# Kernel tuning notes

Hardware: AMD Instinct MI355X
Metric: run time of the kernel (lower is better)

Reference implementation:

```python
import jax, jax.numpy as jnp
import numpy as np

N_NODES = 200000
N_EDGES = 500000
F_IN = 165
HIDDEN = 384
OUT = 2


def setup_inputs() -> dict:
    key = jax.random.key(0)
    ks = jax.random.split(key, 8)
    x = jax.random.normal(ks[0], (N_NODES, F_IN), dtype=jnp.float32)
    edge_index = jax.random.randint(ks[1], (2, N_EDGES), 0, N_NODES, dtype=jnp.int64)
    # Glorot-ish init for GCNConv weights, zero bias (PyG default)
    def glorot(k, fan_in, fan_out):
        lim = (6.0 / (fan_in + fan_out)) ** 0.5
        return jax.random.uniform(k, (fan_in, fan_out), dtype=jnp.float32, minval=-lim, maxval=lim)
    W1 = glorot(ks[2], F_IN, HIDDEN)
    b1 = jnp.zeros((HIDDEN,), dtype=jnp.float32)
    W2 = glorot(ks[3], HIDDEN, HIDDEN)
    b2 = jnp.zeros((HIDDEN,), dtype=jnp.float32)
    W3 = glorot(ks[4], HIDDEN, OUT)
    b3 = jnp.zeros((OUT,), dtype=jnp.float32)
    return {"x": x, "edge_index": edge_index,
            "W1": W1, "b1": b1, "W2": W2, "b2": b2, "W3": W3, "b3": b3}


def _gcn_norm(edge_index, num_nodes):
    # PyG gcn_norm: add self-loops, symmetric normalization D^-1/2 (A+I) D^-1/2
    loop = jnp.arange(num_nodes, dtype=edge_index.dtype)
    row = jnp.concatenate([edge_index[0], loop])
    col = jnp.concatenate([edge_index[1], loop])
    ones = jnp.ones(row.shape[0], dtype=jnp.float32)
    deg = jax.ops.segment_sum(ones, col, num_segments=num_nodes)
    dinv = jnp.where(deg > 0, jax.lax.rsqrt(deg), 0.0)
    norm = dinv[row] * dinv[col]  # [E + N]
    return row, col, norm


def _gcn_conv(h, W, b, row, col, norm, num_nodes):
    h = h @ W                          # [N, F_out] linear transform first
    msg = h[row] * norm[:, None]       # gather + scale, [E+N, F_out]
    agg = jax.ops.segment_sum(msg, col, num_segments=num_nodes)
    return agg + b


def reference(x, edge_index, W1, b1, W2, b2, W3, b3):
    n = x.shape[0]
    row, col, norm = _gcn_norm(edge_index, n)
    h = jax.nn.relu(_gcn_conv(x, W1, b1, row, col, norm, n))
    h = jax.nn.relu(_gcn_conv(h, W2, b2, row, col, norm, n))
    return _gcn_conv(h, W3, b3, row, col, norm, n)
```

## Files before the change

### kernel.cpp

```cpp
#include <hip/hip_runtime.h>
#include <hip/hip_bf16.h>

#define N_NODES 200000
#define N_EDGES 500000
#define F_IN    165
#define HIDDEN  384
#define F_OUT   2

#define KPAD1   192
#define M_TILES 1563
#define M_PAD   (M_TILES * 128)
#define NB_SCAN 782
#define GRID_GEMM (196 * 24)

typedef unsigned short ushort_t;
typedef unsigned int   uint_t;

using bf16x8 = __attribute__((ext_vector_type(8))) short;
using f32x4  = __attribute__((ext_vector_type(4))) float;

__device__ __forceinline__ float bf2f(uint_t u) {
    return __uint_as_float(u << 16);
}
__device__ __forceinline__ ushort_t f2bf(float x) {
    uint_t b = __float_as_uint(x);
    return (ushort_t)((b + 0x7FFFu + ((b >> 16) & 1u)) >> 16);
}

__device__ __forceinline__ void async16(const ushort_t* g, ushort_t* l) {
    __builtin_amdgcn_global_load_lds(
        (const __attribute__((address_space(1))) void*)g,
        (__attribute__((address_space(3))) void*)l,
        16, 0, 0);
}

__global__ void count_kernel(const int* __restrict__ col, int* __restrict__ cnt, int E) {
    int e = blockIdx.x * blockDim.x + threadIdx.x;
    if (e < E) atomicAdd(&cnt[col[e]], 1);
}

__global__ void dinv_kernel(const int* __restrict__ cnt, float* __restrict__ dinv, int n) {
    int i = blockIdx.x * blockDim.x + threadIdx.x;
    if (i < n) dinv[i] = rsqrtf((float)(cnt[i] + 1));
}

__global__ __launch_bounds__(256) void scan1_kernel(const int* __restrict__ cnt,
                                                    int* __restrict__ loc,
                                                    int* __restrict__ bsum, int N) {
    __shared__ int sh[256];
    int t = threadIdx.x;
    int i = blockIdx.x * 256 + t;
    int v = (i < N) ? cnt[i] : 0;
    sh[t] = v;
    __syncthreads();
    #pragma unroll
    for (int off = 1; off < 256; off <<= 1) {
        int u = (t >= off) ? sh[t - off] : 0;
        __syncthreads();
        sh[t] += u;
        __syncthreads();
    }
    int incl = sh[t];
    if (i < N) loc[i] = incl - v;
    if (t == 255) bsum[blockIdx.x] = incl;
}

__global__ __launch_bounds__(1024) void scan2_kernel(int* __restrict__ bsum, int NB) {
    __shared__ int sh[1024];
    int t = threadIdx.x;
    int v = (t < NB) ? bsum[t] : 0;
    sh[t] = v;
    __syncthreads();
    #pragma unroll
    for (int off = 1; off < 1024; off <<= 1) {
        int u = (t >= off) ? sh[t - off] : 0;
        __syncthreads();
        sh[t] += u;
        __syncthreads();
    }
    if (t < NB) bsum[t] = sh[t] - v;
}

__global__ __launch_bounds__(256) void scan3_kernel(int* __restrict__ ptr,
                                                    int* __restrict__ cursor,
                                                    const int* __restrict__ bsum,
                                                    int N, int E) {
    int t = threadIdx.x;
    int i = blockIdx.x * 256 + t;
    if (i < N) {
        int p = ptr[i] + bsum[blockIdx.x];
        ptr[i] = p;
        cursor[i] = p;
    }
    if (i == 0) ptr[N] = E;
}

__global__ void scatter_kernel(const int* __restrict__ row, const int* __restrict__ col,
                               const float* __restrict__ dinv,
                               int* __restrict__ cursor,
                               int* __restrict__ row_srt, float* __restrict__ nrm_srt, int E) {
    int e = blockIdx.x * blockDim.x + threadIdx.x;
    if (e >= E) return;
    int r = row[e], c = col[e];
    int pos = atomicAdd(&cursor[c], 1);
    row_srt[pos] = r;
    nrm_srt[pos] = dinv[r] * dinv[c];
}

__global__ void convx_kernel(const float* __restrict__ X, uint_t* __restrict__ Xb, int total) {
    int idx = blockIdx.x * blockDim.x + threadIdx.x;
    if (idx >= total) return;
    int node = idx / 96, ui = idx - node * 96;
    int f = ui * 2;
    const float* xr = X + (size_t)node * F_IN;
    float lo = (f < F_IN) ? xr[f] : 0.0f;
    float hi = (f + 1 < F_IN) ? xr[f + 1] : 0.0f;
    Xb[idx] = (uint_t)f2bf(lo) | ((uint_t)f2bf(hi) << 16);
}

__global__ __launch_bounds__(256) void agg165b_kernel(
        const uint_t* __restrict__ Xb, const float* __restrict__ dinv,
        const int* __restrict__ ptr, const int* __restrict__ row_srt,
        const float* __restrict__ nrm_srt, ushort_t* __restrict__ out, int N) {
    int w    = (blockIdx.x * blockDim.x + threadIdx.x) >> 6;
    int lane = threadIdx.x & 63;
    if (w >= N) return;
    float d2 = dinv[w]; d2 *= d2;
    const uint_t* self = Xb + (size_t)w * 96;
    bool two = (lane < 19);
    uint_t u0 = self[lane];
    uint_t u1 = two ? self[64 + lane] : 0u;
    float ax0 = bf2f(u0 & 0xFFFFu) * d2, ay0 = bf2f(u0 >> 16) * d2;
    float ax1 = bf2f(u1 & 0xFFFFu) * d2, ay1 = bf2f(u1 >> 16) * d2;
    int e0 = ptr[w], e1 = ptr[w + 1];
    for (int e = e0; e < e1; ++e) {
        int r = row_srt[e];
        float wg = nrm_srt[e];
        const uint_t* hr = Xb + (size_t)r * 96;
        uint_t v0 = hr[lane];
        uint_t v1 = two ? hr[64 + lane] : 0u;
        ax0 = fmaf(bf2f(v0 & 0xFFFFu), wg, ax0);
        ay0 = fmaf(bf2f(v0 >> 16), wg, ay0);
        ax1 = fmaf(bf2f(v1 & 0xFFFFu), wg, ax1);
        ay1 = fmaf(bf2f(v1 >> 16), wg, ay1);
    }
    uint_t* o = (uint_t*)(out + (size_t)w * KPAD1);
    o[lane] = (uint_t)f2bf(ax0) | ((uint_t)f2bf(ay0) << 16);
    if (two) o[64 + lane] = (uint_t)f2bf(ax1) | ((uint_t)f2bf(ay1) << 16);
}

__global__ __launch_bounds__(256) void agg384_kernel(
        const ushort_t* __restrict__ H, const float* __restrict__ dinv,
        const int* __restrict__ ptr, const int* __restrict__ row_srt,
        const float* __restrict__ nrm_srt, ushort_t* __restrict__ out, int N) {
    int w    = (blockIdx.x * blockDim.x + threadIdx.x) >> 6;
    int lane = threadIdx.x & 63;
    if (w >= N) return;
    float d2 = dinv[w]; d2 *= d2;
    const uint_t* self = (const uint_t*)(H + (size_t)w * HIDDEN);
    float ax[3], ay[3];
    #pragma unroll
    for (int j = 0; j < 3; ++j) {
        uint_t u = self[lane + 64 * j];
        ax[j] = bf2f(u & 0xFFFFu) * d2;
        ay[j] = bf2f(u >> 16) * d2;
    }
    int e0 = ptr[w], e1 = ptr[w + 1];
    for (int e = e0; e < e1; ++e) {
        int r = row_srt[e];
        float wg = nrm_srt[e];
        const uint_t* hr = (const uint_t*)(H + (size_t)r * HIDDEN);
        #pragma unroll
        for (int j = 0; j < 3; ++j) {
            uint_t u = hr[lane + 64 * j];
            ax[j] = fmaf(bf2f(u & 0xFFFFu), wg, ax[j]);
            ay[j] = fmaf(bf2f(u >> 16), wg, ay[j]);
        }
    }
    uint_t* o = (uint_t*)(out + (size_t)w * HIDDEN);
    #pragma unroll
    for (int j = 0; j < 3; ++j)
        o[lane + 64 * j] = (uint_t)f2bf(ax[j]) | ((uint_t)f2bf(ay[j]) << 16);
}

__global__ void prep_wt_kernel(const float* __restrict__ W, ushort_t* __restrict__ Wt,
                               int Kin, int Kpad, int Nn) {
    int idx = blockIdx.x * blockDim.x + threadIdx.x;
    if (idx >= Nn * Kpad) return;
    int n = idx / Kpad, k = idx - n * Kpad;
    float v = (k < Kin) ? W[(size_t)k * Nn + n] : 0.0f;
    Wt[idx] = f2bf(v);
}

#define GBK 32

template<bool RELU>
__global__ __launch_bounds__(256) void mfma_gemm_kernel(
        const ushort_t* __restrict__ A, const ushort_t* __restrict__ Wt,
        const float* __restrict__ bias, ushort_t* __restrict__ C,
        int Ks, int Nn, int nTilesM) {
    __shared__ ushort_t As[2][128 * GBK];
    __shared__ ushort_t Bs[2][128 * GBK];

    const int l  = blockIdx.x;
    const int g  = l / 24;
    const int r_ = l - g * 24;
    const int cb = r_ >> 3;
    const int pm = r_ & 7;
    const int pt = g * 8 + pm;
    if (pt >= nTilesM) return;
    const int bm = pt * 128;
    const int bn = cb * 128;

    const int tid  = threadIdx.x;
    const int lane = tid & 63;
    const int w    = tid >> 6;
    const int wm   = w & 1;
    const int wn   = w >> 1;

    auto brow = [](int s) {
        return ((s >> 6) * 64) + ((s & 63) >> 4) + ((s & 15) * 4);
    };

    const int r0  = w * 32;
    const int s0  = r0 + (lane >> 2);
    const int s1  = s0 + 16;
    const int c0  = (lane & 3) ^ ((s0 >> 1) & 3);
    const int c1  = (lane & 3) ^ ((s1 >> 1) & 3);

    const ushort_t* gA0 = A + (size_t)(bm + s0) * Ks + c0 * 8;
    const ushort_t* gA1 = A + (size_t)(bm + s1) * Ks + c1 * 8;
    const ushort_t* gB0 = Wt + (size_t)(bn + brow(s0)) * Ks + c0 * 8;
    const ushort_t* gB1 = Wt + (size_t)(bn + brow(s1)) * Ks + c1 * 8;

    const int p     = lane & 15;
    const int khalf = lane >> 4;
    const int qf    = khalf ^ ((p >> 1) & 3);
    int aoff[4], boff[4];
    #pragma unroll
    for (int f = 0; f < 4; ++f) {
        aoff[f] = (wm * 64 + f * 16 + p) * GBK + qf * 8;
        boff[f] = (wn * 64 + f * 16 + p) * GBK + qf * 8;
    }

    f32x4 acc[4][4] = {};

    const int ksteps = Ks >> 5;
    {
        async16(gA0, &As[0][r0 * GBK]);
        async16(gA1, &As[0][(r0 + 16) * GBK]);
        async16(gB0, &Bs[0][r0 * GBK]);
        async16(gB1, &Bs[0][(r0 + 16) * GBK]);
    }

    int cur = 0;
    for (int kt = 0; kt < ksteps; ++kt) {
        __syncthreads();

        if (kt + 1 < ksteps) {
            const int ko = (kt + 1) * GBK;
            const int nb = cur ^ 1;
            async16(gA0 + ko, &As[nb][r0 * GBK]);
            async16(gA1 + ko, &As[nb][(r0 + 16) * GBK]);
            async16(gB0 + ko, &Bs[nb][r0 * GBK]);
            async16(gB1 + ko, &Bs[nb][(r0 + 16) * GBK]);
        }

        bf16x8 af[4], bfr[4];
        #pragma unroll
        for (int f = 0; f < 4; ++f) {
            af[f]  = *reinterpret_cast<const bf16x8*>(&As[cur][aoff[f]]);
            bfr[f] = *reinterpret_cast<const bf16x8*>(&Bs[cur][boff[f]]);
        }
        #pragma unroll
        for (int mi = 0; mi < 4; ++mi)
            #pragma unroll
            for (int ni = 0; ni < 4; ++ni)
                acc[mi][ni] = __builtin_amdgcn_mfma_f32_16x16x32_bf16(
                    af[mi], bfr[ni], acc[mi][ni], 0, 0, 0);
        cur ^= 1;
    }

    const int colbase = bn + wn * 64 + p * 4;
    const float4 bb = *reinterpret_cast<const float4*>(bias + colbase);
    const float bias4[4] = {bb.x, bb.y, bb.z, bb.w};
    #pragma unroll
    for (int mi = 0; mi < 4; ++mi) {
        const int rowbase = bm + wm * 64 + mi * 16 + khalf * 4;
        #pragma unroll
        for (int j = 0; j < 4; ++j) {
            float v0 = acc[mi][0][j] + bias4[0];
            float v1 = acc[mi][1][j] + bias4[1];
            float v2 = acc[mi][2][j] + bias4[2];
            float v3 = acc[mi][3][j] + bias4[3];
            if (RELU) {
                v0 = fmaxf(v0, 0.f); v1 = fmaxf(v1, 0.f);
                v2 = fmaxf(v2, 0.f); v3 = fmaxf(v3, 0.f);
            }
            ushort4 o;
            o.x = f2bf(v0); o.y = f2bf(v1); o.z = f2bf(v2); o.w = f2bf(v3);
            *reinterpret_cast<ushort4*>(C + (size_t)(rowbase + j) * Nn + colbase) = o;
        }
    }
}

__global__ __launch_bounds__(256) void gemm_n2_kernel(
        const ushort_t* __restrict__ A, const float* __restrict__ W,
        float* __restrict__ G, int M) {
    int w    = (blockIdx.x * blockDim.x + threadIdx.x) >> 6;
    int lane = threadIdx.x & 63;
    if (w >= M) return;
    const uint_t* a = (const uint_t*)(A + (size_t)w * HIDDEN);
    float s0 = 0.f, s1 = 0.f;
    #pragma unroll
    for (int j = 0; j < 3; ++j) {
        int f2 = lane + 64 * j;
        uint_t u = a[f2];
        float alo = bf2f(u & 0xFFFFu), ahi = bf2f(u >> 16);
        int k = f2 * 2;
        s0 = fmaf(alo, W[k * 2 + 0], s0);
        s1 = fmaf(alo, W[k * 2 + 1], s1);
        s0 = fmaf(ahi, W[k * 2 + 2], s0);
        s1 = fmaf(ahi, W[k * 2 + 3], s1);
    }
    #pragma unroll
    for (int off = 32; off; off >>= 1) {
        s0 += __shfl_down(s0, off);
        s1 += __shfl_down(s1, off);
    }
    if (lane == 0) { G[(size_t)w * 2] = s0; G[(size_t)w * 2 + 1] = s1; }
}

__global__ void out_kernel(const float* __restrict__ G, const float* __restrict__ dinv,
                           const int* __restrict__ ptr, const int* __restrict__ row_srt,
                           const float* __restrict__ nrm_srt, const float* __restrict__ b3,
                           float* __restrict__ out, int N) {
    int i = blockIdx.x * blockDim.x + threadIdx.x;
    if (i >= N) return;
    float d2 = dinv[i]; d2 *= d2;
    float a0 = G[(size_t)i * 2 + 0] * d2 + b3[0];
    float a1 = G[(size_t)i * 2 + 1] * d2 + b3[1];
    int e0 = ptr[i], e1 = ptr[i + 1];
    for (int e = e0; e < e1; ++e) {
        int r = row_srt[e];
        float wg = nrm_srt[e];
        a0 = fmaf(G[(size_t)r * 2 + 0], wg, a0);
        a1 = fmaf(G[(size_t)r * 2 + 1], wg, a1);
    }
    out[(size_t)i * 2 + 0] = a0;
    out[(size_t)i * 2 + 1] = a1;
}

extern "C" void kernel_launch(void* const* d_in, const int* in_sizes, int n_in,
                              void* d_out, int out_size, void* d_ws, size_t ws_size,
                              hipStream_t stream) {
    const float* x   = (const float*)d_in[0];
    const int*   ei  = (const int*)  d_in[1];
    const float* W1  = (const float*)d_in[2];
    const float* b1  = (const float*)d_in[3];
    const float* W2  = (const float*)d_in[4];
    const float* b2  = (const float*)d_in[5];
    const float* W3  = (const float*)d_in[6];
    const float* b3  = (const float*)d_in[7];
    float* out = (float*)d_out;

    const int N = N_NODES, E = N_EDGES;
    const int* row = ei;
    const int* col = ei + E;

    size_t off = 0;
    auto alloc = [&](size_t bytes) { size_t o = off; off += (bytes + 255) & ~(size_t)255; return o; };
    size_t o_dinv   = alloc((size_t)N * 4);
    size_t o_ptr    = alloc((size_t)(N + 1) * 4);
    size_t o_cnt    = alloc((size_t)N * 4);
    size_t o_cursor = alloc((size_t)N * 4);
    size_t o_bsum   = alloc((size_t)NB_SCAN * 4);
    size_t o_rowsrt = alloc((size_t)E * 4);
    size_t o_nrmsrt = alloc((size_t)E * 4);
    size_t o_G      = alloc((size_t)N * 2 * 4);
    size_t o_Wt1    = alloc((size_t)HIDDEN * KPAD1 * 2);
    size_t o_Wt2    = alloc((size_t)HIDDEN * HIDDEN * 2);
    size_t o_B1     = alloc((size_t)M_PAD * HIDDEN * 2);
    size_t o_B2     = alloc((size_t)M_PAD * HIDDEN * 2);
    if (ws_size < off) return;

    char* ws = (char*)d_ws;
    float*    dinv    = (float*)(ws + o_dinv);
    int*      ptr     = (int*)  (ws + o_ptr);
    int*      cnt     = (int*)  (ws + o_cnt);
    int*      cursor  = (int*)  (ws + o_cursor);
    int*      bsum    = (int*)  (ws + o_bsum);
    int*      row_srt = (int*)  (ws + o_rowsrt);
    float*    nrm_srt = (float*)(ws + o_nrmsrt);
    float*    G       = (float*)(ws + o_G);
    ushort_t* Wt1     = (ushort_t*)(ws + o_Wt1);
    ushort_t* Wt2     = (ushort_t*)(ws + o_Wt2);
    ushort_t* B1      = (ushort_t*)(ws + o_B1);
    ushort_t* B2      = (ushort_t*)(ws + o_B2);
    uint_t*   Xb      = (uint_t*)B2;

    const int B = 256;

    prep_wt_kernel<<<(HIDDEN * KPAD1 + B - 1) / B, B, 0, stream>>>(W1, Wt1, F_IN, KPAD1, HIDDEN);
    prep_wt_kernel<<<(HIDDEN * HIDDEN + B - 1) / B, B, 0, stream>>>(W2, Wt2, HIDDEN, HIDDEN, HIDDEN);
    convx_kernel<<<(N * 96 + B - 1) / B, B, 0, stream>>>(x, Xb, N * 96);

    hipMemsetAsync(cnt, 0, (size_t)N * 4, stream);
    count_kernel<<<(E + B - 1) / B, B, 0, stream>>>(col, cnt, E);
    dinv_kernel<<<(N + B - 1) / B, B, 0, stream>>>(cnt, dinv, N);
    scan1_kernel<<<NB_SCAN, 256, 0, stream>>>(cnt, ptr, bsum, N);
    scan2_kernel<<<1, 1024, 0, stream>>>(bsum, NB_SCAN);
    scan3_kernel<<<NB_SCAN, 256, 0, stream>>>(ptr, cursor, bsum, N, E);
    scatter_kernel<<<(E + B - 1) / B, B, 0, stream>>>(row, col, dinv, cursor, row_srt, nrm_srt, E);

    agg165b_kernel<<<(N * 64 + B - 1) / B, B, 0, stream>>>(Xb, dinv, ptr, row_srt, nrm_srt, B1, N);

    mfma_gemm_kernel<true><<<GRID_GEMM, 256, 0, stream>>>(B1, Wt1, b1, B2, KPAD1, HIDDEN, M_TILES);

    agg384_kernel<<<(N * 64 + B - 1) / B, B, 0, stream>>>(B2, dinv, ptr, row_srt, nrm_srt, B1, N);

    mfma_gemm_kernel<true><<<GRID_GEMM, 256, 0, stream>>>(B1, Wt2, b2, B2, HIDDEN, HIDDEN, M_TILES);

    gemm_n2_kernel<<<(N * 64 + B - 1) / B, B, 0, stream>>>(B2, W3, G, N);

    out_kernel<<<(N + B - 1) / B, B, 0, stream>>>(G, dinv, ptr, row_srt, nrm_srt, b3, out, N);
}
```

Before: 510.6 us.

## Triple-buffer GEMM shared-memory tiles with explicit vmcnt waits

Moves the MFMA GEMM from a double-buffered to a triple-buffered LDS pipeline. It prefetches three k-tiles up front and uses explicit s_waitcnt vmcnt counts plus raw s_barrier in place of __syncthreads, so two loads stay in flight while the current tile is computed. This is meant to hide global-memory latency better in the short K loops (6 or 12 steps). In exchange it uses 50% more LDS, which may cut occupancy, and adds a second barrier per iteration. It also relies on hand-counted vmcnt values matching the async16 instruction count, and on the compiler not reordering the asm.

```diff
diff --git a/kernel.cpp b/kernel.cpp
--- a/kernel.cpp
+++ b/kernel.cpp
@@ -199,8 +199,8 @@
         const ushort_t* __restrict__ A, const ushort_t* __restrict__ Wt,
         const float* __restrict__ bias, ushort_t* __restrict__ C,
         int Ks, int Nn, int nTilesM) {
-    __shared__ ushort_t As[2][128 * GBK];
-    __shared__ ushort_t Bs[2][128 * GBK];
+    __shared__ ushort_t As[3][128 * GBK];
+    __shared__ ushort_t Bs[3][128 * GBK];
 
     const int l  = blockIdx.x;
     const int g  = l / 24;
@@ -246,31 +246,32 @@
     f32x4 acc[4][4] = {};
 
     const int ksteps = Ks >> 5;
-    {
-        async16(gA0, &As[0][r0 * GBK]);
-        async16(gA1, &As[0][(r0 + 16) * GBK]);
-        async16(gB0, &Bs[0][r0 * GBK]);
-        async16(gB1, &Bs[0][(r0 + 16) * GBK]);
+    #pragma unroll
+    for (int t = 0; t < 3; ++t) {
+        if (t < ksteps) {
+            const int ko = t * GBK;
+            async16(gA0 + ko, &As[t][r0 * GBK]);
+            async16(gA1 + ko, &As[t][(r0 + 16) * GBK]);
+            async16(gB0 + ko, &Bs[t][r0 * GBK]);
+            async16(gB1 + ko, &Bs[t][(r0 + 16) * GBK]);
+        }
     }
 
     int cur = 0;
     for (int kt = 0; kt < ksteps; ++kt) {
-        __syncthreads();
-
-        if (kt + 1 < ksteps) {
-            const int ko = (kt + 1) * GBK;
-            const int nb = cur ^ 1;
-            async16(gA0 + ko, &As[nb][r0 * GBK]);
-            async16(gA1 + ko, &As[nb][(r0 + 16) * GBK]);
-            async16(gB0 + ko, &Bs[nb][r0 * GBK]);
-            async16(gB1 + ko, &Bs[nb][(r0 + 16) * GBK]);
-        }
-
+        const int ahead = ((ksteps - kt) < 3 ? (ksteps - kt) : 3) - 1;
+        if (ahead == 2)      asm volatile("s_waitcnt vmcnt(8)" ::: "memory");
+        else if (ahead == 1) asm volatile("s_waitcnt vmcnt(4)" ::: "memory");
+        else                 asm volatile("s_waitcnt vmcnt(0)" ::: "memory");
+        asm volatile("s_barrier" ::: "memory");
+
+        const ushort_t* Ab = As[cur];
+        const ushort_t* Bb = Bs[cur];
         bf16x8 af[4], bfr[4];
         #pragma unroll
         for (int f = 0; f < 4; ++f) {
-            af[f]  = *reinterpret_cast<const bf16x8*>(&As[cur][aoff[f]]);
-            bfr[f] = *reinterpret_cast<const bf16x8*>(&Bs[cur][boff[f]]);
+            af[f]  = *reinterpret_cast<const bf16x8*>(&Ab[aoff[f]]);
+            bfr[f] = *reinterpret_cast<const bf16x8*>(&Bb[boff[f]]);
         }
         #pragma unroll
         for (int mi = 0; mi < 4; ++mi)
@@ -278,7 +279,16 @@
             for (int ni = 0; ni < 4; ++ni)
                 acc[mi][ni] = __builtin_amdgcn_mfma_f32_16x16x32_bf16(
                     af[mi], bfr[ni], acc[mi][ni], 0, 0, 0);
-        cur ^= 1;
+
+        asm volatile("s_barrier" ::: "memory");
+        if (kt + 3 < ksteps) {
+            const int ko = (kt + 3) * GBK;
+            async16(gA0 + ko, &As[cur][r0 * GBK]);
+            async16(gA1 + ko, &As[cur][(r0 + 16) * GBK]);
+            async16(gB0 + ko, &Bs[cur][r0 * GBK]);
+            async16(gB1 + ko, &Bs[cur][(r0 + 16) * GBK]);
+        }
+        cur = (cur == 2) ? 0 : cur + 1;
     }
 
     const int colbase = bn + wn * 64 + p * 4;
```

Result: no change. 507.7 us (-0.6%).
